# Kernel optimization log

Hardware: AMD Instinct MI355X
Metric: run time of the kernel (lower is better)

Reference implementation:

```python
import jax, jax.numpy as jnp
import numpy as np

B = 96   # batch (must equal C for the residual broadcast to be legal)
C = 96   # num_channels == seq_len (x is (B, C, 1, C))
S = 96   # sequence length = C
NH = 8   # num_heads
DK = 96  # d_k (defaults to num_channels)
G = 8    # groupnorm groups
EPS = 1e-5


def setup_inputs() -> dict:
    key = jax.random.key(0)
    ks = jax.random.split(key, 9)
    D = NH * DK
    scale = 0.05
    return {
        "x": jax.random.normal(ks[0], (B, C, 1, C), jnp.float32),
        "Wq": jax.random.normal(ks[1], (C, D), jnp.float32) * scale,
        "bq": jax.random.normal(ks[2], (D,), jnp.float32) * scale,
        "Wk": jax.random.normal(ks[3], (C, D), jnp.float32) * scale,
        "bk": jax.random.normal(ks[4], (D,), jnp.float32) * scale,
        "Wv": jax.random.normal(ks[5], (C, D), jnp.float32) * scale,
        "bv": jax.random.normal(ks[6], (D,), jnp.float32) * scale,
        "Wo": jax.random.normal(ks[7], (D, C), jnp.float32) * scale,
        "bo": jax.random.normal(ks[8], (C,), jnp.float32) * scale,
        "gamma": jnp.ones((C,), jnp.float32),
        "beta": jnp.zeros((C,), jnp.float32),
    }


def group_norm(x, gamma, beta):
    # x: (B, C, H, W); normalize over (C//G, H, W) within each of G groups
    b, c, h, w = x.shape
    xg = x.reshape(b, G, -1)
    mu = jnp.mean(xg, axis=-1, keepdims=True)
    var = jnp.var(xg, axis=-1, keepdims=True)
    xn = ((xg - mu) * jax.lax.rsqrt(var + EPS)).reshape(b, c, h, w)
    return xn * gamma[None, :, None, None] + beta[None, :, None, None]


def reference(x, Wq, bq, Wk, bk, Wv, bv, Wo, bo, gamma, beta):
    xn = group_norm(x, gamma, beta)           # (B, C, 1, C)
    residual = xn
    t = xn.reshape(B, S, C)                   # H == 1, squeeze
    # self-attention: q = k = v = normalized x
    q = (t @ Wq + bq).reshape(B, S, NH, DK).transpose(0, 2, 1, 3)  # (B, H, S, Dk)
    k = (t @ Wk + bk).reshape(B, S, NH, DK).transpose(0, 2, 1, 3)
    v = (t @ Wv + bv).reshape(B, S, NH, DK).transpose(0, 2, 1, 3)
    scores = jnp.einsum('bhqd,bhkd->bhqk', q, k) / jnp.sqrt(jnp.float32(DK))
    causal = jnp.tril(jnp.ones((S, S), bool))  # mask=True -> causal tril mask
    scores = jnp.where(causal[None, None], scores, -jnp.inf)
    attn = jax.nn.softmax(scores, axis=-1)
    out = jnp.einsum('bhqk,bhkd->bhqd', attn, v)       # (B, H, S, Dk)
    out = out.transpose(0, 2, 1, 3).reshape(B, S, NH * DK)
    out = out @ Wo + bo                                # (B, S, C); dropout(p=0) = id
    # faithful to the source: (B,S,C) + (B,C,1,C) broadcasts to (B,C,S,C)
    return out + residual
```

## Files before the change

kernel.cpp:

```cpp
#include <hip/hip_runtime.h>
#include <hip/hip_bf16.h>

#define BATCH 96
#define CH    96
#define SEQ   96
#define NHEAD 8
#define DK    96
#define DMODEL 768
#define GRP   8
#define EPSV  1e-5f

typedef __bf16 bf16x8 __attribute__((ext_vector_type(8)));
typedef float  f32x4  __attribute__((ext_vector_type(4)));
typedef unsigned short u16;

#define MFMA16(a, b, c) __builtin_amdgcn_mfma_f32_16x16x32_bf16((a), (b), (c), 0, 0, 0)

__device__ __forceinline__ u16 f2bf(float f) {
    union { float f; unsigned int u; } c; c.f = f;
    unsigned int u = c.u + 0x7fffu + ((c.u >> 16) & 1u);
    return (u16)(u >> 16);
}

__global__ __launch_bounds__(128) void prep_kernel(
        const float* __restrict__ x, const float* __restrict__ gamma,
        const float* __restrict__ beta,
        const float* __restrict__ Wq, const float* __restrict__ Wk,
        const float* __restrict__ Wv, const float* __restrict__ Wo,
        float* __restrict__ xn, u16* __restrict__ xn_bf,
        u16* __restrict__ WqT, u16* __restrict__ WkT,
        u16* __restrict__ WvT, u16* __restrict__ WoT) {
    if (blockIdx.x < 768) {
        int bg = blockIdx.x;
        int b = bg >> 3, g = bg & 7;
        const float* xp = x + b * 9216 + g * 1152;
        float vals[9];
        float s = 0.f, ss = 0.f;
        #pragma unroll
        for (int r = 0; r < 9; ++r) {
            float v = xp[threadIdx.x + 128 * r];
            vals[r] = v; s += v; ss += v * v;
        }
        #pragma unroll
        for (int off = 32; off > 0; off >>= 1) {
            s  += __shfl_down(s, off);
            ss += __shfl_down(ss, off);
        }
        __shared__ float red[4];
        if ((threadIdx.x & 63) == 0) {
            red[(threadIdx.x >> 6) * 2]     = s;
            red[(threadIdx.x >> 6) * 2 + 1] = ss;
        }
        __syncthreads();
        s = red[0] + red[2]; ss = red[1] + red[3];
        float mu   = s * (1.0f / 1152.0f);
        float var  = ss * (1.0f / 1152.0f) - mu * mu;
        float rsig = rsqrtf(var + EPSV);
        #pragma unroll
        for (int r = 0; r < 9; ++r) {
            int e = threadIdx.x + 128 * r;
            int c = g * 12 + e / 96;
            float v = (vals[r] - mu) * rsig * gamma[c] + beta[c];
            int idx = b * 9216 + g * 1152 + e;
            xn[idx]    = v;
            xn_bf[idx] = f2bf(v);
        }
    } else {
        int t = blockIdx.x - 768;
        int seg = t / 576;
        int idx = (t - seg * 576) * 128 + threadIdx.x;
        const float* src = seg == 0 ? Wq : seg == 1 ? Wk : seg == 2 ? Wv : Wo;
        u16* dst = seg == 0 ? WqT : seg == 1 ? WkT : seg == 2 ? WvT : WoT;
        if (seg < 3) {
            int n = idx / 96, k2 = idx - n * 96;
            dst[idx] = f2bf(src[k2 * 768 + n]);
        } else {
            int n = idx / 768, k2 = idx - n * 768;
            dst[idx] = f2bf(src[k2 * 96 + n]);
        }
    }
}

__global__ __launch_bounds__(384) void fattn_kernel(
        const u16* __restrict__ xn_bf,
        const u16* __restrict__ WqT, const u16* __restrict__ WkT,
        const u16* __restrict__ WvT,
        const float* __restrict__ bq, const float* __restrict__ bk,
        const float* __restrict__ bv,
        u16* __restrict__ attn_out) {
    int b = blockIdx.x >> 3, h = blockIdx.x & 7;
    __shared__ __align__(16) u16 qb[96][104];
    __shared__ __align__(16) u16 kb[96][104];
    __shared__ __align__(16) u16 vt[96][104];

    int wave = threadIdx.x >> 6, lane = threadIdx.x & 63;
    int ln = lane & 15, quad = lane >> 4;
    int m0 = wave * 16;
    const u16* xb = xn_bf + b * 9216;
    const int hq = h * 96;

    bf16x8 a[3], av[3];
    #pragma unroll
    for (int kt = 0; kt < 3; ++kt) {
        a[kt]  = *(const bf16x8*)(xb + (m0 + ln) * 96 + kt * 32 + quad * 8);
        av[kt] = *(const bf16x8*)(WvT + (hq + m0 + ln) * 96 + kt * 32 + quad * 8);
    }
    f32x4 aq[6] = {}, ak[6] = {}, avv[6] = {};
    #pragma unroll
    for (int kt = 0; kt < 3; ++kt) {
        #pragma unroll
        for (int nt = 0; nt < 6; ++nt) {
            bf16x8 bqf = *(const bf16x8*)(WqT + (hq + nt * 16 + ln) * 96 + kt * 32 + quad * 8);
            aq[nt] = MFMA16(a[kt], bqf, aq[nt]);
            bf16x8 bkf = *(const bf16x8*)(WkT + (hq + nt * 16 + ln) * 96 + kt * 32 + quad * 8);
            ak[nt] = MFMA16(a[kt], bkf, ak[nt]);
            bf16x8 bvf = *(const bf16x8*)(xb + (nt * 16 + ln) * 96 + kt * 32 + quad * 8);
            avv[nt] = MFMA16(av[kt], bvf, avv[nt]);
        }
    }
    float bvr[4];
    #pragma unroll
    for (int r = 0; r < 4; ++r) bvr[r] = bv[hq + m0 + quad * 4 + r];
    #pragma unroll
    for (int nt = 0; nt < 6; ++nt) {
        int col = nt * 16 + ln;
        float bqc = bq[hq + col], bkc = bk[hq + col];
        #pragma unroll
        for (int r = 0; r < 4; ++r) {
            int row = m0 + quad * 4 + r;
            qb[row][col] = f2bf(aq[nt][r] + bqc);
            kb[row][col] = f2bf(ak[nt][r] + bkc);
            vt[row][col] = f2bf(avv[nt][r] + bvr[r]);
        }
    }
    __syncthreads();

    f32x4 accs[6] = {};
    #pragma unroll
    for (int kt = 0; kt < 3; ++kt) {
        bf16x8 aa = *(const bf16x8*)(&qb[m0 + ln][kt * 32 + quad * 8]);
        #pragma unroll
        for (int nt = 0; nt < 6; ++nt) {
            bf16x8 bb = *(const bf16x8*)(&kb[nt * 16 + ln][kt * 32 + quad * 8]);
            accs[nt] = MFMA16(aa, bb, accs[nt]);
        }
    }

    const float scale = 0.10206207261596577f;
    float pout[4][6];
    #pragma unroll
    for (int r = 0; r < 4; ++r) {
        int row = m0 + quad * 4 + r;
        float vals[6], m = -1e30f;
        #pragma unroll
        for (int nt = 0; nt < 6; ++nt) {
            int col = nt * 16 + ln;
            float sv = accs[nt][r] * scale;
            vals[nt] = (col <= row) ? sv : -1e30f;
            m = fmaxf(m, vals[nt]);
        }
        #pragma unroll
        for (int off = 1; off < 16; off <<= 1) m = fmaxf(m, __shfl_xor(m, off));
        float sum = 0.f;
        #pragma unroll
        for (int nt = 0; nt < 6; ++nt) {
            float p = (vals[nt] > -1e29f) ? __expf(vals[nt] - m) : 0.f;
            pout[r][nt] = p; sum += p;
        }
        #pragma unroll
        for (int off = 1; off < 16; off <<= 1) sum += __shfl_xor(sum, off);
        float rinv = 1.0f / sum;
        #pragma unroll
        for (int nt = 0; nt < 6; ++nt) pout[r][nt] *= rinv;
    }
    __syncthreads();
    #pragma unroll
    for (int r = 0; r < 4; ++r)
        #pragma unroll
        for (int nt = 0; nt < 6; ++nt)
            kb[m0 + quad * 4 + r][nt * 16 + ln] = f2bf(pout[r][nt]);
    __syncthreads();

    f32x4 acco[6] = {};
    #pragma unroll
    for (int kt = 0; kt < 3; ++kt) {
        bf16x8 aa = *(const bf16x8*)(&kb[m0 + ln][kt * 32 + quad * 8]);
        #pragma unroll
        for (int nt = 0; nt < 6; ++nt) {
            bf16x8 bb = *(const bf16x8*)(&vt[nt * 16 + ln][kt * 32 + quad * 8]);
            acco[nt] = MFMA16(aa, bb, acco[nt]);
        }
    }
    const size_t obase = (size_t)b * 96 * DMODEL + hq;
    #pragma unroll
    for (int nt = 0; nt < 6; ++nt) {
        int d = nt * 16 + ln;
        #pragma unroll
        for (int r = 0; r < 4; ++r) {
            int row = m0 + quad * 4 + r;
            attn_out[obase + (size_t)row * DMODEL + d] = f2bf(acco[nt][r]);
        }
    }
}

__global__ __launch_bounds__(256) void obcast_kernel(
        const u16* __restrict__ attn, const u16* __restrict__ WoT,
        const float* __restrict__ bo, const float* __restrict__ xn,
        float* __restrict__ out) {
    __shared__ __align__(16) float red[4][16][96];
    __shared__ __align__(16) float xnt[96][96];
    int wave = threadIdx.x >> 6, lane = threadIdx.x & 63;
    int ln = lane & 15, quad = lane >> 4;
    int m0 = blockIdx.x * 16;
    int j  = blockIdx.x / 6;
    int k0 = (blockIdx.x - j * 6) * 16;

    {
        const f32x4* xn4 = (const f32x4*)xn;
        f32x4* xt4 = (f32x4*)xnt;
        #pragma unroll
        for (int it = 0; it < 9; ++it) {
            int idx = threadIdx.x + it * 256;
            int i = idx / 24, l4 = idx - i * 24;
            xt4[idx] = xn4[(size_t)(i * 96 + j) * 24 + l4];
        }
    }

    int kw = wave * 192;
    f32x4 acc[6] = {};
    #pragma unroll
    for (int kt = 0; kt < 6; ++kt) {
        bf16x8 a = *(const bf16x8*)(attn + (size_t)(m0 + ln) * DMODEL + kw + kt * 32 + quad * 8);
        #pragma unroll
        for (int nt = 0; nt < 6; ++nt) {
            bf16x8 bb = *(const bf16x8*)(WoT + (nt * 16 + ln) * DMODEL + kw + kt * 32 + quad * 8);
            acc[nt] = MFMA16(a, bb, acc[nt]);
        }
    }
    #pragma unroll
    for (int nt = 0; nt < 6; ++nt)
        #pragma unroll
        for (int r = 0; r < 4; ++r)
            red[wave][quad * 4 + r][nt * 16 + ln] = acc[nt][r];
    __syncthreads();

    #pragma unroll
    for (int e = 0; e < 6; ++e) {
        int idx = threadIdx.x + e * 256;
        int row = idx / 96, col = idx - row * 96;
        red[0][row][col] = red[0][row][col] + red[1][row][col] +
                           red[2][row][col] + red[3][row][col] + bo[col];
    }
    __syncthreads();

    f32x4* out4 = (f32x4*)out;
    const f32x4* pt4 = (const f32x4*)red;
    const f32x4* xt4 = (const f32x4*)xnt;
    #pragma unroll 4
    for (int it = 0; it < 144; ++it) {
        int idx = threadIdx.x + it * 256;
        int i = idx / 384;
        int rem = idx - i * 384;
        int k = rem / 24, l4 = rem - k * 24;
        f32x4 pv = pt4[k * 24 + l4];
        f32x4 xv = xt4[i * 24 + l4];
        f32x4 rr = pv + xv;
        __builtin_nontemporal_store(rr,
            &out4[((size_t)(i * 96 + j) * 96 + (k0 + k)) * 24 + l4]);
    }
}

extern "C" void kernel_launch(void* const* d_in, const int* in_sizes, int n_in,
                              void* d_out, int out_size, void* d_ws, size_t ws_size,
                              hipStream_t stream) {
    const float* x     = (const float*)d_in[0];
    const float* Wq    = (const float*)d_in[1];
    const float* bq    = (const float*)d_in[2];
    const float* Wk    = (const float*)d_in[3];
    const float* bk    = (const float*)d_in[4];
    const float* Wv    = (const float*)d_in[5];
    const float* bv    = (const float*)d_in[6];
    const float* Wo    = (const float*)d_in[7];
    const float* bo    = (const float*)d_in[8];
    const float* gamma = (const float*)d_in[9];
    const float* beta  = (const float*)d_in[10];
    float* out = (float*)d_out;

    char* ws = (char*)d_ws;
    float* xn_f = (float*)(ws + 0);
    u16*  xn_b  = (u16*)(ws + 3538944);
    u16*  WqT   = (u16*)(ws + 5308416);
    u16*  WkT   = (u16*)(ws + 5455872);
    u16*  WvT   = (u16*)(ws + 5603328);
    u16*  WoT   = (u16*)(ws + 5750784);
    u16*  ab    = (u16*)(ws + 5898240);

    prep_kernel<<<dim3(3072), dim3(128), 0, stream>>>(
        x, gamma, beta, Wq, Wk, Wv, Wo, xn_f, xn_b, WqT, WkT, WvT, WoT);
    fattn_kernel<<<dim3(BATCH * NHEAD), dim3(384), 0, stream>>>(
        xn_b, WqT, WkT, WvT, bq, bk, bv, ab);
    obcast_kernel<<<dim3(576), dim3(256), 0, stream>>>(ab, WoT, bo, xn_f, out);
}
```

Before: 415.7 us.

## Split broadcast output kernel across i-quarters with six-wave K-split

The output/broadcast kernel now launches four times as many blocks. Each block covers a quarter of the broadcast i dimension, and the Wo GEMM reduction is split over six waves instead of four. Each thread keeps one projected row segment in registers and streams 24 strided nontemporal stores, with a smaller shared-memory xn tile. This aims to raise parallelism and occupancy on the store-bound 340MB output write, but it recomputes the small Wo GEMM four times per tile.

```diff
diff --git a/kernel.cpp b/kernel.cpp
--- a/kernel.cpp
+++ b/kernel.cpp
@@ -203,33 +203,40 @@
     }
 }
 
-__global__ __launch_bounds__(256) void obcast_kernel(
+__global__ __launch_bounds__(384) void obcast_kernel(
         const u16* __restrict__ attn, const u16* __restrict__ WoT,
         const float* __restrict__ bo, const float* __restrict__ xn,
         float* __restrict__ out) {
-    __shared__ __align__(16) float red[4][16][96];
-    __shared__ __align__(16) float xnt[96][96];
+    __shared__ __align__(16) float red[6][16][96];
+    __shared__ __align__(16) float xnt[24][96];
     int wave = threadIdx.x >> 6, lane = threadIdx.x & 63;
     int ln = lane & 15, quad = lane >> 4;
-    int m0 = blockIdx.x * 16;
-    int j  = blockIdx.x / 6;
-    int k0 = (blockIdx.x - j * 6) * 16;
+
+    int bid = blockIdx.x;
+    int iq = bid & 3;
+    int jk = bid >> 2;
+    int j  = jk / 6;
+    int k0 = (jk - j * 6) * 16;
+    int m0 = jk * 16;
+    int i0 = iq * 24;
 
     {
         const f32x4* xn4 = (const f32x4*)xn;
         f32x4* xt4 = (f32x4*)xnt;
-        #pragma unroll
-        for (int it = 0; it < 9; ++it) {
-            int idx = threadIdx.x + it * 256;
-            int i = idx / 24, l4 = idx - i * 24;
-            xt4[idx] = xn4[(size_t)(i * 96 + j) * 24 + l4];
-        }
-    }
-
-    int kw = wave * 192;
+        int idx = threadIdx.x;
+        int i = idx / 24, l4 = idx - i * 24;
+        xt4[idx] = xn4[(size_t)((i0 + i) * 96 + j) * 24 + l4];
+        if (threadIdx.x < 192) {
+            int idx2 = threadIdx.x + 384;
+            int i2 = idx2 / 24, l42 = idx2 - i2 * 24;
+            xt4[idx2] = xn4[(size_t)((i0 + i2) * 96 + j) * 24 + l42];
+        }
+    }
+
+    int kw = wave * 128;
     f32x4 acc[6] = {};
     #pragma unroll
-    for (int kt = 0; kt < 6; ++kt) {
+    for (int kt = 0; kt < 4; ++kt) {
         bf16x8 a = *(const bf16x8*)(attn + (size_t)(m0 + ln) * DMODEL + kw + kt * 32 + quad * 8);
         #pragma unroll
         for (int nt = 0; nt < 6; ++nt) {
@@ -245,28 +252,27 @@
     __syncthreads();
 
     #pragma unroll
-    for (int e = 0; e < 6; ++e) {
-        int idx = threadIdx.x + e * 256;
+    for (int e = 0; e < 4; ++e) {
+        int idx = threadIdx.x + e * 384;
         int row = idx / 96, col = idx - row * 96;
         red[0][row][col] = red[0][row][col] + red[1][row][col] +
-                           red[2][row][col] + red[3][row][col] + bo[col];
+                           red[2][row][col] + red[3][row][col] +
+                           red[4][row][col] + red[5][row][col] + bo[col];
     }
     __syncthreads();
 
     f32x4* out4 = (f32x4*)out;
     const f32x4* pt4 = (const f32x4*)red;
     const f32x4* xt4 = (const f32x4*)xnt;
-    #pragma unroll 4
-    for (int it = 0; it < 144; ++it) {
-        int idx = threadIdx.x + it * 256;
-        int i = idx / 384;
-        int rem = idx - i * 384;
-        int k = rem / 24, l4 = rem - k * 24;
-        f32x4 pv = pt4[k * 24 + l4];
-        f32x4 xv = xt4[i * 24 + l4];
-        f32x4 rr = pv + xv;
-        __builtin_nontemporal_store(rr,
-            &out4[((size_t)(i * 96 + j) * 96 + (k0 + k)) * 24 + l4]);
+    int k  = threadIdx.x / 24;
+    int l4 = threadIdx.x - k * 24;
+    f32x4 pv = pt4[k * 24 + l4];
+    size_t o = ((size_t)(i0 * 96 + j) * 96 + (k0 + k)) * 24 + l4;
+    #pragma unroll
+    for (int i = 0; i < 24; ++i) {
+        f32x4 rr = pv + xt4[i * 24 + l4];
+        __builtin_nontemporal_store(rr, &out4[o]);
+        o += 221184;
     }
 }
 
@@ -299,5 +305,5 @@
         x, gamma, beta, Wq, Wk, Wv, Wo, xn_f, xn_b, WqT, WkT, WvT, WoT);
     fattn_kernel<<<dim3(BATCH * NHEAD), dim3(384), 0, stream>>>(
         xn_b, WqT, WkT, WvT, bq, bk, bv, ab);
-    obcast_kernel<<<dim3(576), dim3(256), 0, stream>>>(ab, WoT, bo, xn_f, out);
-}
+    obcast_kernel<<<dim3(2304), dim3(384), 0, stream>>>(ab, WoT, bo, xn_f, out);
+}
```

Result: no change. 413.7 us (-0.5%).
